# Performance work log

Hardware: AMD Instinct MI355X
Metric: run time of the kernel (lower is better)

The kernel has to match this reference:

```python
import jax, jax.numpy as jnp
import numpy as np

N, D = 16384, 16     # nodes (hits), node feature dim (= embedding dim, slice is full)
K = 64               # max_num_neighbors
MAX_RADIUS = 6.0     # kNN radius cut
PID_MAX = 5000


def setup_inputs() -> dict:
    key = jax.random.key(0)
    k1, k2 = jax.random.split(key)
    x = jax.random.normal(k1, (N, D), dtype=jnp.float32)
    particle_id = jax.random.randint(k2, (N,), 0, PID_MAX, dtype=jnp.int32)
    return {"x": x, "particle_id": particle_id}


def reference(x, particle_id):
    # ml is None and embedding_slice=(None,None) -> embedding features are x itself
    emb = x
    # knn_graph: squared pairwise distances, self-loops excluded (diag = +inf)
    sq = jnp.sum(emb * emb, axis=1)                       # [N]
    d2 = sq[:, None] + sq[None, :] - 2.0 * (emb @ emb.T)  # [N, N]
    diag = jnp.arange(N)
    d2 = d2.at[diag, diag].set(jnp.inf)
    _, nbr = jax.lax.top_k(-d2, K)                        # [N, K] nearest neighbor ids
    src = nbr.reshape(-1)                                 # edge_index[0]: neighbor (source)
    dst = jnp.repeat(jnp.arange(N, dtype=src.dtype), K)   # edge_index[1]: query node
    # radius filter: keep edges with dist < max_radius (fixed shape -> boolean mask)
    diff = x[src] - x[dst]                                # [N*K, D]
    dists = jnp.sqrt(jnp.maximum(jnp.sum(diff * diff, axis=1), 0.0))
    mask = dists < MAX_RADIUS                             # [N*K]
    # edge truth labels: same (nonzero) particle id on both ends
    y = (particle_id[src] == particle_id[dst]) & (particle_id[src] > 0) & mask
    # edge features: [x_src - x_dst, x_src + x_dst], zeroed on masked-out edges
    edge_features = jnp.concatenate([diff, x[src] + x[dst]], axis=1)
    edge_features = edge_features * mask[:, None].astype(x.dtype)
    edge_index = jnp.stack([src, dst])                    # [2, N*K]
    return x, edge_index, y.astype(jnp.int32), edge_features, mask
```

## Files before the change

kernel.cpp:

```cpp
#include <hip/hip_runtime.h>

#define NN 16384
#define DD 16
#define KK 64
#define QQ 4
#define TPB 512
#define HIST 1024
#define LIST_MAX 1024
#define CAND_MAX 256

__device__ __forceinline__ float halving_sumsq16(const float* v) {
    float p[16];
#pragma unroll
    for (int d = 0; d < 16; ++d) p[d] = __fmul_rn(v[d], v[d]);
    float r8[8];
#pragma unroll
    for (int j = 0; j < 8; ++j) r8[j] = __fadd_rn(p[j], p[j + 8]);
    float r4[4];
#pragma unroll
    for (int j = 0; j < 4; ++j) r4[j] = __fadd_rn(r8[j], r8[j + 4]);
    float r2[2];
#pragma unroll
    for (int j = 0; j < 2; ++j) r2[j] = __fadd_rn(r4[j], r4[j + 2]);
    return __fadd_rn(r2[0], r2[1]);
}

__device__ __forceinline__ float d2_of(const float* xi, const float* xj,
                                       float sqi, float sqj) {
    float dot = 0.0f;
#pragma unroll
    for (int d = 0; d < DD; ++d) dot = fmaf(xi[d], xj[d], dot);
    return __fsub_rn(__fadd_rn(sqi, sqj), __fmul_rn(2.0f, dot));
}

__device__ __forceinline__ int bucket_of(float d2) {
    int b = (int)__fmul_rn(d2, 4.0f);
    if (b < 0) b = 0;
    if (b >= HIST) b = HIST - 1;
    return b;
}

__global__ void prep_kernel(const float* __restrict__ x,
                            float* __restrict__ out_x,
                            float* __restrict__ sqf) {
    int i = blockIdx.x * blockDim.x + threadIdx.x;
    if (i < NN) {
        float v[DD];
#pragma unroll
        for (int d = 0; d < DD; ++d) v[d] = x[i * DD + d];
        sqf[i] = halving_sumsq16(v);
    }
    for (int t = i; t < NN * DD; t += gridDim.x * blockDim.x) {
        out_x[t] = x[t];
    }
}

__global__ __launch_bounds__(TPB, 4) void knn_kernel(
        const float* __restrict__ x,
        const int* __restrict__ pid,
        const float* __restrict__ sqf,
        float* __restrict__ out_src,
        float* __restrict__ out_dst,
        float* __restrict__ out_y,
        float* __restrict__ out_ef,
        float* __restrict__ out_mask) {
    __shared__ unsigned int hist[QQ][HIST];
    __shared__ unsigned short list[QQ][LIST_MAX];
    __shared__ unsigned int cand_key[QQ][CAND_MAX];
    __shared__ int cand_idx[QQ][CAND_MAX];
    __shared__ unsigned int wavesum[QQ][TPB / 64];
    __shared__ int s_bsel[QQ];
    __shared__ unsigned int s_listcnt[QQ], s_candcnt[QQ];
    __shared__ int s_fb[QQ];

    const int bid = blockIdx.x;
    const int tid = threadIdx.x;
    const int lane = tid & 63;
    const int w = tid >> 6;
    const int iA = bid * QQ;

    for (int t = tid; t < QQ * HIST; t += TPB)
        ((unsigned int*)hist)[t] = 0;
    if (tid < QQ) { s_listcnt[tid] = 0; s_candcnt[tid] = 0; s_bsel[tid] = HIST - 1; }

    float xq[QQ][DD];
    float sq[QQ], Tq[QQ];
#pragma unroll
    for (int q = 0; q < QQ; ++q) {
        const float4* p = reinterpret_cast<const float4*>(x + (iA + q) * DD);
        float4 a0 = p[0], a1 = p[1], a2 = p[2], a3 = p[3];
        xq[q][0]=a0.x; xq[q][1]=a0.y; xq[q][2]=a0.z; xq[q][3]=a0.w;
        xq[q][4]=a1.x; xq[q][5]=a1.y; xq[q][6]=a1.z; xq[q][7]=a1.w;
        xq[q][8]=a2.x; xq[q][9]=a2.y; xq[q][10]=a2.z; xq[q][11]=a2.w;
        xq[q][12]=a3.x; xq[q][13]=a3.y; xq[q][14]=a3.z; xq[q][15]=a3.w;
        sq[q] = sqf[iA + q];
        Tq[q] = 16.0f + sq[q] - 1.8f * sqrtf(32.0f + 4.0f * sq[q]);
    }
    __syncthreads();

    for (int j = tid; j < NN; j += TPB) {
        const float4* xj4 = reinterpret_cast<const float4*>(x + j * DD);
        float4 a0 = xj4[0], a1 = xj4[1], a2 = xj4[2], a3 = xj4[3];
        float xj[DD] = {a0.x, a0.y, a0.z, a0.w, a1.x, a1.y, a1.z, a1.w,
                        a2.x, a2.y, a2.z, a2.w, a3.x, a3.y, a3.z, a3.w};
        const float sj = sqf[j];
#pragma unroll
        for (int q = 0; q < QQ; ++q) {
            float d2 = d2_of(xq[q], xj, sq[q], sj);
            if (d2 < Tq[q] && j != iA + q) {
                unsigned int pos = atomicAdd(&s_listcnt[q], 1u);
                if (pos < LIST_MAX) list[q][pos] = (unsigned short)j;
            }
        }
    }
    __syncthreads();

    if (tid < QQ)
        s_fb[tid] = (s_listcnt[tid] < KK) || (s_listcnt[tid] > LIST_MAX);
    __syncthreads();
    const int anyfb = s_fb[0] | s_fb[1] | s_fb[2] | s_fb[3];

    if (anyfb) {
        for (int j = tid; j < NN; j += TPB) {
            const float4* xj4 = reinterpret_cast<const float4*>(x + j * DD);
            float4 a0 = xj4[0], a1 = xj4[1], a2 = xj4[2], a3 = xj4[3];
            float xj[DD] = {a0.x, a0.y, a0.z, a0.w, a1.x, a1.y, a1.z, a1.w,
                            a2.x, a2.y, a2.z, a2.w, a3.x, a3.y, a3.z, a3.w};
            const float sj = sqf[j];
#pragma unroll
            for (int q = 0; q < QQ; ++q) {
                if (s_fb[q] && j != iA + q) {
                    float d2 = d2_of(xq[q], xj, sq[q], sj);
                    atomicAdd(&hist[q][bucket_of(d2)], 1u);
                }
            }
        }
    }

#pragma unroll
    for (int q = 0; q < QQ; ++q) {
        if (!s_fb[q]) {
            const int lc = (int)s_listcnt[q];
            for (int e = tid; e < lc; e += TPB) {
                const int j = list[q][e];
                const float4* xj4 = reinterpret_cast<const float4*>(x + j * DD);
                float4 a0 = xj4[0], a1 = xj4[1], a2 = xj4[2], a3 = xj4[3];
                float xj[DD] = {a0.x, a0.y, a0.z, a0.w, a1.x, a1.y, a1.z, a1.w,
                                a2.x, a2.y, a2.z, a2.w, a3.x, a3.y, a3.z, a3.w};
                float d2 = d2_of(xq[q], xj, sq[q], sqf[j]);
                atomicAdd(&hist[q][bucket_of(d2)], 1u);
            }
        }
    }
    __syncthreads();

    {
        unsigned int local[QQ], inc[QQ];
#pragma unroll
        for (int q = 0; q < QQ; ++q) {
            const int b0 = tid * (HIST / TPB);
            unsigned int s = 0;
#pragma unroll
            for (int b = 0; b < HIST / TPB; ++b) s += hist[q][b0 + b];
            local[q] = s;
            unsigned int v = s;
#pragma unroll
            for (int off = 1; off < 64; off <<= 1) {
                unsigned int n = __shfl_up(v, off, 64);
                if (lane >= off) v += n;
            }
            inc[q] = v;
        }
        if (lane == 63)
#pragma unroll
            for (int q = 0; q < QQ; ++q) wavesum[q][w] = inc[q];
        __syncthreads();
#pragma unroll
        for (int q = 0; q < QQ; ++q) {
            unsigned int woff = 0;
            for (int ww = 0; ww < w; ++ww) woff += wavesum[q][ww];
            unsigned int cum = inc[q] + woff;
            unsigned int prev = cum - local[q];
            if (prev < KK && KK <= cum) {
                unsigned int acc = prev;
                int b = tid * (HIST / TPB);
                while (acc + hist[q][b] < KK) { acc += hist[q][b]; ++b; }
                s_bsel[q] = b;
            }
        }
    }
    __syncthreads();

#pragma unroll
    for (int q = 0; q < QQ; ++q) {
        if (!s_fb[q]) {
            const int bsel = s_bsel[q];
            const int lc = (int)s_listcnt[q];
            for (int e = tid; e < lc; e += TPB) {
                const int j = list[q][e];
                const float4* xj4 = reinterpret_cast<const float4*>(x + j * DD);
                float4 a0 = xj4[0], a1 = xj4[1], a2 = xj4[2], a3 = xj4[3];
                float xj[DD] = {a0.x, a0.y, a0.z, a0.w, a1.x, a1.y, a1.z, a1.w,
                                a2.x, a2.y, a2.z, a2.w, a3.x, a3.y, a3.z, a3.w};
                float d2 = d2_of(xq[q], xj, sq[q], sqf[j]);
                if (bucket_of(d2) <= bsel) {
                    unsigned int pos = atomicAdd(&s_candcnt[q], 1u);
                    if (pos < CAND_MAX) {
                        unsigned int u = __float_as_uint(d2);
                        u ^= (u & 0x80000000u) ? 0xFFFFFFFFu : 0x80000000u;
                        cand_key[q][pos] = u;
                        cand_idx[q][pos] = j;
                    }
                }
            }
        }
    }
    if (anyfb) {
        for (int j = tid; j < NN; j += TPB) {
            const float4* xj4 = reinterpret_cast<const float4*>(x + j * DD);
            float4 a0 = xj4[0], a1 = xj4[1], a2 = xj4[2], a3 = xj4[3];
            float xj[DD] = {a0.x, a0.y, a0.z, a0.w, a1.x, a1.y, a1.z, a1.w,
                            a2.x, a2.y, a2.z, a2.w, a3.x, a3.y, a3.z, a3.w};
            const float sj = sqf[j];
#pragma unroll
            for (int q = 0; q < QQ; ++q) {
                if (s_fb[q] && j != iA + q) {
                    float d2 = d2_of(xq[q], xj, sq[q], sj);
                    if (bucket_of(d2) <= s_bsel[q]) {
                        unsigned int pos = atomicAdd(&s_candcnt[q], 1u);
                        if (pos < CAND_MAX) {
                            unsigned int u = __float_as_uint(d2);
                            u ^= (u & 0x80000000u) ? 0xFFFFFFFFu : 0x80000000u;
                            cand_key[q][pos] = u;
                            cand_idx[q][pos] = j;
                        }
                    }
                }
            }
        }
    }
    __syncthreads();

    for (int q = 0; q < QQ; ++q) {
        const int iq = iA + q;
        const int mypid = pid[iq];
        int c = (int)s_candcnt[q];
        if (c > CAND_MAX) c = CAND_MAX;
        for (int t = tid; t < c; t += TPB) {
            const unsigned int kt = cand_key[q][t];
            const int jt = cand_idx[q][t];
            int rank = 0;
            for (int u = 0; u < c; ++u) {
                unsigned int ku = cand_key[q][u];
                rank += (ku < kt) || (ku == kt && cand_idx[q][u] < jt);
            }
            if (rank < KK) {
                const long e = (long)iq * KK + rank;
                out_src[e] = (float)jt;

                const float* xj = x + jt * DD;
                float diff[DD], sum[DD];
#pragma unroll
                for (int d = 0; d < DD; ++d) {
                    float a = xj[d], b = xq[q][d];
                    diff[d] = __fsub_rn(a, b);
                    sum[d]  = __fadd_rn(a, b);
                }
                const float s2 = halving_sumsq16(diff);
                const bool m = __fsqrt_rn(s2) < 6.0f;
                out_mask[e] = m ? 1.0f : 0.0f;
                const int pj = pid[jt];
                out_y[e] = (m && pj == mypid && pj > 0) ? 1.0f : 0.0f;

                float* ef = out_ef + e * (2 * DD);
#pragma unroll
                for (int d = 0; d < DD; ++d) ef[d] = m ? diff[d] : 0.0f;
#pragma unroll
                for (int d = 0; d < DD; ++d) ef[DD + d] = m ? sum[d] : 0.0f;
            }
        }
    }

    for (int t = tid; t < QQ * KK; t += TPB) {
        out_dst[(long)iA * KK + t] = (float)(iA + t / KK);
    }
}

extern "C" void kernel_launch(void* const* d_in, const int* in_sizes, int n_in,
                              void* d_out, int out_size, void* d_ws, size_t ws_size,
                              hipStream_t stream) {
    const float* x = (const float*)d_in[0];
    const int* pid = (const int*)d_in[1];
    float* out = (float*)d_out;

    float* out_x   = out;
    float* out_src = out_x + NN * DD;
    float* out_dst = out_src + NN * KK;
    float* out_y   = out_dst + NN * KK;
    float* out_ef  = out_y + NN * KK;
    float* out_mask = out_ef + (long)NN * KK * 2 * DD;

    float* sqf = (float*)d_ws;

    prep_kernel<<<NN / 256, 256, 0, stream>>>(x, out_x, sqf);
    knn_kernel<<<NN / QQ, TPB, 0, stream>>>(x, pid, sqf, out_src, out_dst,
                                            out_y, out_ef, out_mask);
}
```

Measured before the change: 427.1 us.

## Halve block size, pack histogram into 16-bit counters, aggregate list appends per wave

The kNN kernel now runs 256-thread blocks without the min-blocks launch bound. The histogram is packed as two 16-bit counters per 32-bit word, halving its shared memory footprint. List appends in the candidate scan go through a wave-level ballot and a single leader atomic instead of one atomic per lane. The self-exclusion test moves out of the hot scan and into the candidate stage, so thresholds are shifted by one to account for the self entry. The goal is less shared-atomic contention and more resident blocks, at the risk of 16-bit counter overflow and more complex bucket-selection logic.

```diff
diff --git a/kernel.cpp b/kernel.cpp
--- a/kernel.cpp
+++ b/kernel.cpp
@@ -4,8 +4,9 @@
 #define DD 16
 #define KK 64
 #define QQ 4
-#define TPB 512
+#define TPB 256
 #define HIST 1024
+#define HISTW (HIST/2)
 #define LIST_MAX 1024
 #define CAND_MAX 256
 
@@ -55,7 +56,7 @@
     }
 }
 
-__global__ __launch_bounds__(TPB, 4) void knn_kernel(
+__global__ __launch_bounds__(TPB) void knn_kernel(
         const float* __restrict__ x,
         const int* __restrict__ pid,
         const float* __restrict__ sqf,
@@ -64,7 +65,7 @@
         float* __restrict__ out_y,
         float* __restrict__ out_ef,
         float* __restrict__ out_mask) {
-    __shared__ unsigned int hist[QQ][HIST];
+    __shared__ unsigned int hist[QQ][HISTW];
     __shared__ unsigned short list[QQ][LIST_MAX];
     __shared__ unsigned int cand_key[QQ][CAND_MAX];
     __shared__ int cand_idx[QQ][CAND_MAX];
@@ -79,7 +80,7 @@
     const int w = tid >> 6;
     const int iA = bid * QQ;
 
-    for (int t = tid; t < QQ * HIST; t += TPB)
+    for (int t = tid; t < QQ * HISTW; t += TPB)
         ((unsigned int*)hist)[t] = 0;
     if (tid < QQ) { s_listcnt[tid] = 0; s_candcnt[tid] = 0; s_bsel[tid] = HIST - 1; }
 
@@ -107,8 +108,16 @@
 #pragma unroll
         for (int q = 0; q < QQ; ++q) {
             float d2 = d2_of(xq[q], xj, sq[q], sj);
-            if (d2 < Tq[q] && j != iA + q) {
-                unsigned int pos = atomicAdd(&s_listcnt[q], 1u);
+            bool want = d2 < Tq[q];
+            unsigned long long m = __ballot(want);
+            if (want) {
+                int leader = __ffsll(m) - 1;
+                unsigned int base = 0;
+                if (lane == leader)
+                    base = atomicAdd(&s_listcnt[q], (unsigned int)__popcll(m));
+                base = __shfl(base, leader, 64);
+                unsigned int pos =
+                    base + (unsigned int)__popcll(m & ((1ull << lane) - 1ull));
                 if (pos < LIST_MAX) list[q][pos] = (unsigned short)j;
             }
         }
@@ -116,7 +125,7 @@
     __syncthreads();
 
     if (tid < QQ)
-        s_fb[tid] = (s_listcnt[tid] < KK) || (s_listcnt[tid] > LIST_MAX);
+        s_fb[tid] = (s_listcnt[tid] < KK + 1) || (s_listcnt[tid] > LIST_MAX);
     __syncthreads();
     const int anyfb = s_fb[0] | s_fb[1] | s_fb[2] | s_fb[3];
 
@@ -131,7 +140,8 @@
             for (int q = 0; q < QQ; ++q) {
                 if (s_fb[q] && j != iA + q) {
                     float d2 = d2_of(xq[q], xj, sq[q], sj);
-                    atomicAdd(&hist[q][bucket_of(d2)], 1u);
+                    int b = bucket_of(d2);
+                    atomicAdd(&hist[q][b >> 1], 1u << ((b & 1) << 4));
                 }
             }
         }
@@ -148,7 +158,8 @@
                 float xj[DD] = {a0.x, a0.y, a0.z, a0.w, a1.x, a1.y, a1.z, a1.w,
                                 a2.x, a2.y, a2.z, a2.w, a3.x, a3.y, a3.z, a3.w};
                 float d2 = d2_of(xq[q], xj, sq[q], sqf[j]);
-                atomicAdd(&hist[q][bucket_of(d2)], 1u);
+                int b = bucket_of(d2);
+                atomicAdd(&hist[q][b >> 1], 1u << ((b & 1) << 4));
             }
         }
     }
@@ -156,12 +167,14 @@
 
     {
         unsigned int local[QQ], inc[QQ];
+        unsigned int pc0[QQ], pc1[QQ], pc2[QQ], pc3[QQ];
 #pragma unroll
         for (int q = 0; q < QQ; ++q) {
-            const int b0 = tid * (HIST / TPB);
-            unsigned int s = 0;
-#pragma unroll
-            for (int b = 0; b < HIST / TPB; ++b) s += hist[q][b0 + b];
+            unsigned int h0 = hist[q][2 * tid];
+            unsigned int h1 = hist[q][2 * tid + 1];
+            pc0[q] = h0 & 0xFFFFu; pc1[q] = h0 >> 16;
+            pc2[q] = h1 & 0xFFFFu; pc3[q] = h1 >> 16;
+            unsigned int s = pc0[q] + pc1[q] + pc2[q] + pc3[q];
             local[q] = s;
             unsigned int v = s;
 #pragma unroll
@@ -177,14 +190,17 @@
         __syncthreads();
 #pragma unroll
         for (int q = 0; q < QQ; ++q) {
+            const unsigned int need = s_fb[q] ? KK : (KK + 1);
             unsigned int woff = 0;
             for (int ww = 0; ww < w; ++ww) woff += wavesum[q][ww];
             unsigned int cum = inc[q] + woff;
             unsigned int prev = cum - local[q];
-            if (prev < KK && KK <= cum) {
+            if (prev < need && need <= cum) {
                 unsigned int acc = prev;
-                int b = tid * (HIST / TPB);
-                while (acc + hist[q][b] < KK) { acc += hist[q][b]; ++b; }
+                int b = 4 * tid;
+                if (acc + pc0[q] < need) { acc += pc0[q]; ++b;
+                    if (acc + pc1[q] < need) { acc += pc1[q]; ++b;
+                        if (acc + pc2[q] < need) { acc += pc2[q]; ++b; } } }
                 s_bsel[q] = b;
             }
         }
@@ -203,7 +219,7 @@
                 float xj[DD] = {a0.x, a0.y, a0.z, a0.w, a1.x, a1.y, a1.z, a1.w,
                                 a2.x, a2.y, a2.z, a2.w, a3.x, a3.y, a3.z, a3.w};
                 float d2 = d2_of(xq[q], xj, sq[q], sqf[j]);
-                if (bucket_of(d2) <= bsel) {
+                if (bucket_of(d2) <= bsel && j != iA + q) {
                     unsigned int pos = atomicAdd(&s_candcnt[q], 1u);
                     if (pos < CAND_MAX) {
                         unsigned int u = __float_as_uint(d2);
```

Result: faster. 394.4 us (-7.7%).
